# Optimization experiments

Measured on AMD Instinct MI355X. Metric: run time of the kernel, lower is better.

Reference implementation:

```python
import jax, jax.numpy as jnp
import numpy as np

K = 20  # hard-coded neighbor count in the original module


def setup_inputs() -> dict:
    key = jax.random.key(0)
    ks = jax.random.split(key, 7)
    B, C, N = 16, 3, 4096
    return {
        "x": jax.random.normal(ks[0], (B, C, N), dtype=jnp.float32),
        "w1": jax.random.normal(ks[1], (16, 3), dtype=jnp.float32) * 0.3,
        "b1": jax.random.normal(ks[2], (16,), dtype=jnp.float32) * 0.1,
        "w2": jax.random.normal(ks[3], (16, 3), dtype=jnp.float32) * 0.3,
        "b2": jax.random.normal(ks[4], (16,), dtype=jnp.float32) * 0.1,
        "w3": jax.random.normal(ks[5], (1, 16), dtype=jnp.float32) * 0.3,
        "b3": jax.random.normal(ks[6], (1,), dtype=jnp.float32) * 0.1,
    }


def reference(x, w1, b1, w2, b2, w3, b3):
    # x: [B, 3, N]
    B, C, N = x.shape
    xt = jnp.transpose(x, (0, 2, 1))  # [B, N, 3]

    # --- KNN: topk of negative squared pairwise distance (includes self) ---
    xx = jnp.sum(x * x, axis=1)                      # [B, N]
    inner = jnp.einsum('bcn,bcm->bnm', x, x)         # [B, N, N]
    neg_dist = -xx[:, :, None] + 2.0 * inner - xx[:, None, :]
    _, idx = jax.lax.top_k(neg_dist, K)              # [B, N, K]

    # --- neighbor gather ---
    neighbors = jnp.take_along_axis(xt[:, None, :, :], idx[..., None], axis=2)  # [B,N,K,3]
    diff = xt[:, :, None, :] - neighbors             # [B, N, K, 3] (center - neighbor)

    # --- 1x1 conv branches (pointwise matmuls) ---
    f1 = jnp.einsum('bnc,oc->bno', xt, w1) + b1      # conv2d1: [B, N, 16]
    sa = jnp.einsum('bno,po->bnp', f1, w3) + b3      # conv2d3(self): [B, N, 1]
    x1 = jnp.einsum('bnkc,oc->bnko', diff, w2) + b2  # conv2d2: [B, N, K, 16]
    na = jnp.einsum('bnko,o->bnk', x1, w3[0]) + b3[0]  # conv2d3(edge): [B, N, K]

    # --- attention coefficients + aggregation ---
    logits = sa + na                                  # [B, N, K] (sa broadcasts over K)
    coefs = jax.nn.softmax(jax.nn.leaky_relu(logits, 0.01), axis=-1)
    vals = jnp.einsum('bnk,bnko->bno', coefs, x1)     # [B, N, 16]
    ret = jax.nn.elu(vals)
    return jnp.transpose(ret, (0, 2, 1))              # [B, 16, N]
```

## Files before the change

### kernel.cpp

```cpp
#include <hip/hip_runtime.h>
#include <math.h>
#include <float.h>

#define NPTS 4096
#define KNN  20
#define RPW  2
#define WAVES 4
#define ROWSB (WAVES * RPW)
#define NCHUNK (NPTS / 256)

#define ROW_SHR1    0x111
#define ROW_SHR2    0x112
#define ROW_SHR4    0x114
#define ROW_SHR8    0x118
#define ROW_BCAST15 0x142
#define ROW_BCAST31 0x143

template <int CTRL>
__device__ __forceinline__ float dpp_mv(float x, float ident) {
    int r = __builtin_amdgcn_update_dpp(__float_as_int(ident), __float_as_int(x),
                                        CTRL, 0xf, 0xf, false);
    return __int_as_float(r);
}
__device__ __forceinline__ float readlane_f(float v, int l) {
    return __int_as_float(__builtin_amdgcn_readlane(__float_as_int(v), l));
}
__device__ __forceinline__ float wave_min_bcast(float v) {
    v = fminf(v, dpp_mv<ROW_SHR1>(v, FLT_MAX));
    v = fminf(v, dpp_mv<ROW_SHR2>(v, FLT_MAX));
    v = fminf(v, dpp_mv<ROW_SHR4>(v, FLT_MAX));
    v = fminf(v, dpp_mv<ROW_SHR8>(v, FLT_MAX));
    v = fminf(v, dpp_mv<ROW_BCAST15>(v, FLT_MAX));
    v = fminf(v, dpp_mv<ROW_BCAST31>(v, FLT_MAX));
    return readlane_f(v, 63);
}
__device__ __forceinline__ float half_max(float v) {
    v = fmaxf(v, dpp_mv<ROW_SHR1>(v, -FLT_MAX));
    v = fmaxf(v, dpp_mv<ROW_SHR2>(v, -FLT_MAX));
    v = fmaxf(v, dpp_mv<ROW_SHR4>(v, -FLT_MAX));
    v = fmaxf(v, dpp_mv<ROW_SHR8>(v, -FLT_MAX));
    v = fmaxf(v, dpp_mv<ROW_BCAST15>(v, -FLT_MAX));
    return v;
}
__device__ __forceinline__ float half_sum(float v) {
    v += dpp_mv<ROW_SHR1>(v, 0.f);
    v += dpp_mv<ROW_SHR2>(v, 0.f);
    v += dpp_mv<ROW_SHR4>(v, 0.f);
    v += dpp_mv<ROW_SHR8>(v, 0.f);
    v += dpp_mv<ROW_BCAST15>(v, 0.f);
    return v;
}

#define INS_STAGE(cc, ii)                                        \
    { bool lt_ = (v < cc);                                       \
      float mx_ = lt_ ? cc : v;  int mi_ = lt_ ? ii : vi;        \
      cc = lt_ ? v : cc;         ii = lt_ ? vi : ii;             \
      v = mx_; vi = mi_; }

#define INS4(R)  INS_STAGE(q[R][0], ji[R][0]) INS_STAGE(q[R][1], ji[R][1]) \
                 INS_STAGE(q[R][2], ji[R][2]) INS_STAGE(q[R][3], ji[R][3])

#define PROC_CHUNK(PX, PY, PZ, CH)                                      \
    {   const int mbase_ = ((CH) << 8) + (lane << 2);                   \
        _Pragma("unroll")                                               \
        for (int c = 0; c < 4; ++c) {                                   \
            const float mx = PX[c], my = PY[c], mz = PZ[c];             \
            const float mxx = mx*mx + my*my + mz*mz;                    \
            const int mi = mbase_ + c;                                  \
            _Pragma("unroll")                                           \
            for (int r = 0; r < RPW; ++r) {                             \
                float inner = cx[r]*mx + cy[r]*my + cz[r]*mz;           \
                float v = mxx - (2.0f * inner - xx[r]);                 \
                int vi = mi;                                            \
                INS4(r)                                                 \
            }                                                           \
        }                                                               \
    }

#define LOAD_CHUNK(PX, PY, PZ, CH)                                      \
    {   const int f4i_ = (((CH) & (NCHUNK - 1)) << 6) + lane;           \
        *(float4*)PX = g4[f4i_];                                        \
        *(float4*)PY = g4[f4i_ + 1024];                                 \
        *(float4*)PZ = g4[f4i_ + 2048];                                 \
    }

__global__ __launch_bounds__(256, 6)
void lae_kernel(const float* __restrict__ x,
                const float* __restrict__ w1, const float* __restrict__ b1,
                const float* __restrict__ w2, const float* __restrict__ b2,
                const float* __restrict__ w3, const float* __restrict__ b3,
                float* __restrict__ out)
{
    __shared__ int s_nbr[ROWSB][KNN];

    const int tid  = threadIdx.x;
    const int lane = tid & 63;
    const int wid  = tid >> 6;
    const int b    = blockIdx.y;
    const int rbase = blockIdx.x * ROWSB + wid * RPW;

    const float* xb = x + (size_t)b * 3 * NPTS;
    const float4* g4 = (const float4*)xb;

    float cx[RPW], cy[RPW], cz[RPW], xx[RPW];
    #pragma unroll
    for (int r = 0; r < RPW; ++r) {
        cx[r] = xb[rbase + r];
        cy[r] = xb[rbase + r + NPTS];
        cz[r] = xb[rbase + r + 2 * NPTS];
        xx[r] = cx[r]*cx[r] + cy[r]*cy[r] + cz[r]*cz[r];
    }

    float q[RPW][4];
    int   ji[RPW][4];
    #pragma unroll
    for (int r = 0; r < RPW; ++r)
        #pragma unroll
        for (int s = 0; s < 4; ++s) { q[r][s] = FLT_MAX; ji[r][s] = -1; }

    float pxA[4], pyA[4], pzA[4], pxB[4], pyB[4], pzB[4];
    LOAD_CHUNK(pxA, pyA, pzA, 0)
    #pragma unroll 1
    for (int ch = 0; ch < NCHUNK; ch += 2) {
        LOAD_CHUNK(pxB, pyB, pzB, ch + 1)
        PROC_CHUNK(pxA, pyA, pzA, ch)
        LOAD_CHUNK(pxA, pyA, pzA, ch + 2)
        PROC_CHUNK(pxB, pyB, pzB, ch + 1)
    }

    int cnt[RPW] = {4, 4};
    for (int t = 0; t < KNN; ++t) {
        float g[RPW]; int win[RPW]; int midx[RPW];
        #pragma unroll
        for (int r = 0; r < RPW; ++r) g[r] = wave_min_bcast(q[r][0]);
        #pragma unroll
        for (int r = 0; r < RPW; ++r) {
            unsigned long long mk = __ballot(q[r][0] == g[r]);
            win[r]  = (int)__builtin_ctzll(mk);
            midx[r] = __builtin_amdgcn_readlane(ji[r][0], win[r]);
        }
        if (lane == 0) {
            #pragma unroll
            for (int r = 0; r < RPW; ++r) s_nbr[wid * RPW + r][t] = midx[r];
        }
        #pragma unroll
        for (int r = 0; r < RPW; ++r) {
            if (lane == win[r]) {
                q[r][0] = q[r][1]; ji[r][0] = ji[r][1];
                q[r][1] = q[r][2]; ji[r][1] = ji[r][2];
                q[r][2] = q[r][3]; ji[r][2] = ji[r][3];
                q[r][3] = FLT_MAX; ji[r][3] = -1;
                cnt[r]--;
            }
        }
        #pragma unroll
        for (int r = 0; r < RPW; ++r) {
            if (cnt[r] == 0) {
                q[r][0] = FLT_MAX; q[r][1] = FLT_MAX; q[r][2] = FLT_MAX; q[r][3] = FLT_MAX;
                ji[r][0] = -1; ji[r][1] = -1; ji[r][2] = -1; ji[r][3] = -1;
                for (int j = 0; j < 64; ++j) {
                    const int mi = ((j >> 2) << 8) + (lane << 2) + (j & 3);
                    bool ex = false;
                    for (int e = 0; e <= t; ++e)
                        ex = ex || (s_nbr[wid * RPW + r][e] == mi);
                    if (!ex) {
                        float mx = xb[mi], my = xb[mi + NPTS], mz = xb[mi + 2*NPTS];
                        float inner = cx[r]*mx + cy[r]*my + cz[r]*mz;
                        float mxx   = mx*mx + my*my + mz*mz;
                        float v = mxx - (2.0f * inner - xx[r]);
                        int vi = mi;
                        INS4(r)
                    }
                }
                cnt[r] = 4;
            }
        }
    }

    const int  kh    = lane & 31;
    const bool lower = (lane < 32);
    const bool valid = (kh < KNN);
    const int  kk    = valid ? kh : 0;

    const float ex = lower ? cx[0] : cx[1];
    const float ey = lower ? cy[0] : cy[1];
    const float ez = lower ? cz[0] : cz[1];
    const int rib  = wid * RPW + (lower ? 0 : 1);
    const int nrow = rbase + (lower ? 0 : 1);

    float sa = b3[0];
    #pragma unroll
    for (int o = 0; o < 16; ++o) {
        float f = b1[o] + w1[o*3+0]*ex + w1[o*3+1]*ey + w1[o*3+2]*ez;
        sa += w3[o] * f;
    }

    const int m = s_nbr[rib][kk];
    float dx = ex - xb[m], dy = ey - xb[m + NPTS], dz = ez - xb[m + 2*NPTS];
    float x1v[16];
    float na = b3[0];
    #pragma unroll
    for (int o = 0; o < 16; ++o) {
        float t2 = b2[o] + w2[o*3+0]*dx + w2[o*3+1]*dy + w2[o*3+2]*dz;
        x1v[o] = t2;
        na += w3[o] * t2;
    }
    float logit = sa + na;
    float l = (logit >= 0.f) ? logit : 0.01f * logit;

    float hm  = half_max(valid ? l : -FLT_MAX);
    float lm  = lower ? readlane_f(hm, 31) : readlane_f(hm, 63);
    float pr  = valid ? expf(l - lm) : 0.f;
    float hs  = half_sum(pr);
    float ps  = lower ? readlane_f(hs, 31) : readlane_f(hs, 63);
    float coef = pr / ps;

    float res = 0.f;
    #pragma unroll
    for (int o = 0; o < 16; ++o) {
        float s  = half_sum(coef * x1v[o]);
        float sv = lower ? readlane_f(s, 31) : readlane_f(s, 63);
        res = (kh == o) ? sv : res;
    }
    if (kh < 16) {
        float r2 = (res > 0.f) ? res : expm1f(res);
        out[((size_t)b * 16 + kh) * NPTS + nrow] = r2;
    }
}

extern "C" void kernel_launch(void* const* d_in, const int* in_sizes, int n_in,
                              void* d_out, int out_size, void* d_ws, size_t ws_size,
                              hipStream_t stream)
{
    const float* x  = (const float*)d_in[0];
    const float* w1 = (const float*)d_in[1];
    const float* b1 = (const float*)d_in[2];
    const float* w2 = (const float*)d_in[3];
    const float* b2 = (const float*)d_in[4];
    const float* w3 = (const float*)d_in[5];
    const float* b3 = (const float*)d_in[6];
    float* out = (float*)d_out;

    dim3 grid(NPTS / ROWSB, 16, 1);
    lae_kernel<<<grid, dim3(256, 1, 1), 0, stream>>>(x, w1, b1, w2, b2, w3, b3, out);
}
```

Baseline: 339.7 us.

## Process one query row per wave and keep neighbor indices in lanes

Each wave now handles a single query point instead of two, which halves the per-thread top-k register state and the distance work per lane. The grid doubles, so every block streams the whole point cloud once per four rows instead of once per eight. Neighbor indices are held one per lane and read back with readlane instead of going through shared memory. Fewer registers may allow more waves per CU, but total global loads and distance evaluations across the grid roughly double, and half the lanes sit idle in the attention epilogue.

Result: slower. 356.8 us (+5.0%).

```diff
diff --git a/kernel.cpp b/kernel.cpp
--- a/kernel.cpp
+++ b/kernel.cpp
@@ -4,9 +4,8 @@
 
 #define NPTS 4096
 #define KNN  20
-#define RPW  2
 #define WAVES 4
-#define ROWSB (WAVES * RPW)
+#define ROWSB WAVES
 #define NCHUNK (NPTS / 256)
 
 #define ROW_SHR1    0x111
@@ -57,8 +56,7 @@
       cc = lt_ ? v : cc;         ii = lt_ ? vi : ii;             \
       v = mx_; vi = mi_; }
 
-#define INS4(R)  INS_STAGE(q[R][0], ji[R][0]) INS_STAGE(q[R][1], ji[R][1]) \
-                 INS_STAGE(q[R][2], ji[R][2]) INS_STAGE(q[R][3], ji[R][3])
+#define INS4  INS_STAGE(q0, j0) INS_STAGE(q1, j1) INS_STAGE(q2, j2) INS_STAGE(q3, j3)
 
 #define PROC_CHUNK(PX, PY, PZ, CH)                                      \
     {   const int mbase_ = ((CH) << 8) + (lane << 2);                   \
@@ -66,14 +64,10 @@
         for (int c = 0; c < 4; ++c) {                                   \
             const float mx = PX[c], my = PY[c], mz = PZ[c];             \
             const float mxx = mx*mx + my*my + mz*mz;                    \
-            const int mi = mbase_ + c;                                  \
-            _Pragma("unroll")                                           \
-            for (int r = 0; r < RPW; ++r) {                             \
-                float inner = cx[r]*mx + cy[r]*my + cz[r]*mz;           \
-                float v = mxx - (2.0f * inner - xx[r]);                 \
-                int vi = mi;                                            \
-                INS4(r)                                                 \
-            }                                                           \
+            float inner = cx*mx + cy*my + cz*mz;                        \
+            float v = mxx - (2.0f * inner - xx);                        \
+            int vi = mbase_ + c;                                        \
+            INS4                                                        \
         }                                                               \
     }
 
@@ -91,32 +85,22 @@
                 const float* __restrict__ w3, const float* __restrict__ b3,
                 float* __restrict__ out)
 {
-    __shared__ int s_nbr[ROWSB][KNN];
-
     const int tid  = threadIdx.x;
     const int lane = tid & 63;
     const int wid  = tid >> 6;
     const int b    = blockIdx.y;
-    const int rbase = blockIdx.x * ROWSB + wid * RPW;
+    const int nrow = blockIdx.x * ROWSB + wid;
 
     const float* xb = x + (size_t)b * 3 * NPTS;
     const float4* g4 = (const float4*)xb;
 
-    float cx[RPW], cy[RPW], cz[RPW], xx[RPW];
-    #pragma unroll
-    for (int r = 0; r < RPW; ++r) {
-        cx[r] = xb[rbase + r];
-        cy[r] = xb[rbase + r + NPTS];
-        cz[r] = xb[rbase + r + 2 * NPTS];
-        xx[r] = cx[r]*cx[r] + cy[r]*cy[r] + cz[r]*cz[r];
-    }
-
-    float q[RPW][4];
-    int   ji[RPW][4];
-    #pragma unroll
-    for (int r = 0; r < RPW; ++r)
-        #pragma unroll
-        for (int s = 0; s < 4; ++s) { q[r][s] = FLT_MAX; ji[r][s] = -1; }
+    const float cx = xb[nrow];
+    const float cy = xb[nrow + NPTS];
+    const float cz = xb[nrow + 2 * NPTS];
+    const float xx = cx*cx + cy*cy + cz*cz;
+
+    float q0 = FLT_MAX, q1 = FLT_MAX, q2 = FLT_MAX, q3 = FLT_MAX;
+    int   j0 = -1, j1 = -1, j2 = -1, j3 = -1;
 
     float pxA[4], pyA[4], pzA[4], pxB[4], pyB[4], pzB[4];
     LOAD_CHUNK(pxA, pyA, pzA, 0)
@@ -128,75 +112,52 @@
         PROC_CHUNK(pxB, pyB, pzB, ch + 1)
     }
 
-    int cnt[RPW] = {4, 4};
+    int nbr = 0;
+    int cnt = 4;
     for (int t = 0; t < KNN; ++t) {
-        float g[RPW]; int win[RPW]; int midx[RPW];
-        #pragma unroll
-        for (int r = 0; r < RPW; ++r) g[r] = wave_min_bcast(q[r][0]);
-        #pragma unroll
-        for (int r = 0; r < RPW; ++r) {
-            unsigned long long mk = __ballot(q[r][0] == g[r]);
-            win[r]  = (int)__builtin_ctzll(mk);
-            midx[r] = __builtin_amdgcn_readlane(ji[r][0], win[r]);
+        float g = wave_min_bcast(q0);
+        unsigned long long mk = __ballot(q0 == g);
+        int win  = (int)__builtin_ctzll(mk);
+        int midx = __builtin_amdgcn_readlane(j0, win);
+        if (lane == t) nbr = midx;
+        if (lane == win) {
+            q0 = q1; j0 = j1; q1 = q2; j1 = j2; q2 = q3; j2 = j3;
+            q3 = FLT_MAX; j3 = -1;
+            cnt--;
         }
-        if (lane == 0) {
-            #pragma unroll
-            for (int r = 0; r < RPW; ++r) s_nbr[wid * RPW + r][t] = midx[r];
+        if (cnt == 0) {
+            q0 = FLT_MAX; q1 = FLT_MAX; q2 = FLT_MAX; q3 = FLT_MAX;
+            j0 = -1; j1 = -1; j2 = -1; j3 = -1;
+            for (int j = 0; j < 64; ++j) {
+                const int mi = ((j >> 2) << 8) + (lane << 2) + (j & 3);
+                bool ex = false;
+                for (int e = 0; e <= t; ++e)
+                    ex = ex || (__builtin_amdgcn_readlane(nbr, e) == mi);
+                if (!ex) {
+                    float mx = xb[mi], my = xb[mi + NPTS], mz = xb[mi + 2*NPTS];
+                    float inner = cx*mx + cy*my + cz*mz;
+                    float mxx   = mx*mx + my*my + mz*mz;
+                    float v = mxx - (2.0f * inner - xx);
+                    int vi = mi;
+                    INS4
+                }
+            }
+            cnt = 4;
         }
-        #pragma unroll
-        for (int r = 0; r < RPW; ++r) {
-            if (lane == win[r]) {
-                q[r][0] = q[r][1]; ji[r][0] = ji[r][1];
-                q[r][1] = q[r][2]; ji[r][1] = ji[r][2];
-                q[r][2] = q[r][3]; ji[r][2] = ji[r][3];
-                q[r][3] = FLT_MAX; ji[r][3] = -1;
-                cnt[r]--;
-            }
-        }
-        #pragma unroll
-        for (int r = 0; r < RPW; ++r) {
-            if (cnt[r] == 0) {
-                q[r][0] = FLT_MAX; q[r][1] = FLT_MAX; q[r][2] = FLT_MAX; q[r][3] = FLT_MAX;
-                ji[r][0] = -1; ji[r][1] = -1; ji[r][2] = -1; ji[r][3] = -1;
-                for (int j = 0; j < 64; ++j) {
-                    const int mi = ((j >> 2) << 8) + (lane << 2) + (j & 3);
-                    bool ex = false;
-                    for (int e = 0; e <= t; ++e)
-                        ex = ex || (s_nbr[wid * RPW + r][e] == mi);
-                    if (!ex) {
-                        float mx = xb[mi], my = xb[mi + NPTS], mz = xb[mi + 2*NPTS];
-                        float inner = cx[r]*mx + cy[r]*my + cz[r]*mz;
-                        float mxx   = mx*mx + my*my + mz*mz;
-                        float v = mxx - (2.0f * inner - xx[r]);
-                        int vi = mi;
-                        INS4(r)
-                    }
-                }
-                cnt[r] = 4;
-            }
-        }
     }
 
     const int  kh    = lane & 31;
-    const bool lower = (lane < 32);
-    const bool valid = (kh < KNN);
-    const int  kk    = valid ? kh : 0;
-
-    const float ex = lower ? cx[0] : cx[1];
-    const float ey = lower ? cy[0] : cy[1];
-    const float ez = lower ? cz[0] : cz[1];
-    const int rib  = wid * RPW + (lower ? 0 : 1);
-    const int nrow = rbase + (lower ? 0 : 1);
+    const bool valid = (kh < KNN) && (lane < 32);
 
     float sa = b3[0];
     #pragma unroll
     for (int o = 0; o < 16; ++o) {
-        float f = b1[o] + w1[o*3+0]*ex + w1[o*3+1]*ey + w1[o*3+2]*ez;
+        float f = b1[o] + w1[o*3+0]*cx + w1[o*3+1]*cy + w1[o*3+2]*cz;
         sa += w3[o] * f;
     }
 
-    const int m = s_nbr[rib][kk];
-    float dx = ex - xb[m], dy = ey - xb[m + NPTS], dz = ez - xb[m + 2*NPTS];
+    const int m = valid ? nbr : 0;
+    float dx = cx - xb[m], dy = cy - xb[m + NPTS], dz = cz - xb[m + 2*NPTS];
     float x1v[16];
     float na = b3[0];
     #pragma unroll
@@ -209,22 +170,22 @@
     float l = (logit >= 0.f) ? logit : 0.01f * logit;
 
     float hm  = half_max(valid ? l : -FLT_MAX);
-    float lm  = lower ? readlane_f(hm, 31) : readlane_f(hm, 63);
+    float lm  = readlane_f(hm, 31);
     float pr  = valid ? expf(l - lm) : 0.f;
     float hs  = half_sum(pr);
-    float ps  = lower ? readlane_f(hs, 31) : readlane_f(hs, 63);
+    float ps  = readlane_f(hs, 31);
     float coef = pr / ps;
 
     float res = 0.f;
     #pragma unroll
     for (int o = 0; o < 16; ++o) {
         float s  = half_sum(coef * x1v[o]);
-        float sv = lower ? readlane_f(s, 31) : readlane_f(s, 63);
+        float sv = readlane_f(s, 31);
         res = (kh == o) ? sv : res;
     }
-    if (kh < 16) {
+    if (lane < 16) {
         float r2 = (res > 0.f) ? res : expm1f(res);
-        out[((size_t)b * 16 + kh) * NPTS + nrow] = r2;
+        out[((size_t)b * 16 + lane) * NPTS + nrow] = r2;
     }
 }
 
```
